# Optimization experiments

Hardware: AMD Instinct MI355X
Metric: run time of the kernel (lower is better)

## Reference

```python
import jax, jax.numpy as jnp
import numpy as np

DIM = 768
HEADS = 12
HD = DIM // HEADS
SCALE = float(np.sqrt(HD))  # sqrt(dim // num_heads)


def layernorm(x, g, b, eps=1e-5):
    m = jnp.mean(x, axis=-1, keepdims=True)
    v = jnp.var(x, axis=-1, keepdims=True)
    return (x - m) * jax.lax.rsqrt(v + eps) * g + b


def dwconv(x, w, b, pad):
    # x: [B,C,H,W], w: [C,1,kh,kw] depthwise
    y = jax.lax.conv_general_dilated(
        x, w, window_strides=(1, 1), padding=[(pad, pad), (pad, pad)],
        feature_group_count=x.shape[1], dimension_numbers=('NCHW', 'OIHW', 'NCHW'))
    return y + b[None, :, None, None]


def mha(xq, xkv, wq, bq, wk, bk, wv, bv, wo, bo):
    # per-head Linears batched over heads; wq/wk/wv: [H, C, hd], biases [H, hd]
    B, N, C = xq.shape
    q = jnp.einsum('bnc,hcd->bhnd', xq, wq) + bq[None, :, None, :]
    k = jnp.einsum('bnc,hcd->bhnd', xkv, wk) + bk[None, :, None, :]
    v = jnp.einsum('bnc,hcd->bhnd', xkv, wv) + bv[None, :, None, :]
    z = jax.nn.sigmoid(jnp.einsum('bhnd,bhmd->bhnm', q, k) / SCALE)  # sigmoid, not softmax
    o = jnp.einsum('bhnm,bhmd->bhnd', z, v)
    o = o.transpose(0, 2, 1, 3).reshape(B, N, C)  # concat heads along feature dim
    return o @ wo + bo


def reference(decoder, wq1, bq1, wk1, bk1, wv1, bv1, wo1, bo1,
              wq2, bq2, wk2, bk2, wv2, bv2, wo2, bo2,
              alphas1, alphas2, peg_w, peg_b,
              ln1_g, ln1_b, ln2_g, ln2_b,
              cn_dw_w, cn_dw_b, cn_ln_g, cn_ln_b,
              cn_w1, cn_b1, cn_w2, cn_b2, cn_scale, cn_alphas):
    B, C, H, W = decoder.shape
    x = decoder.transpose(0, 2, 3, 1).reshape(B, H * W, C)  # [B,N,C]
    # block 1: alpha * x + MHA(x,x,x)
    x = alphas1 * x + mha(x, x, wq1, bq1, wk1, bk1, wv1, bv1, wo1, bo1)
    # PEG: depthwise 3x3 conv (replaces x, no residual in source)
    x4 = x.reshape(B, H, W, C).transpose(0, 3, 1, 2)
    x4 = dwconv(x4, peg_w, peg_b, pad=1)
    x = x4.transpose(0, 2, 3, 1).reshape(B, H * W, C)
    x = layernorm(x, ln1_g, ln1_b)
    # block 2 (encoder is None -> self-attention)
    x = alphas2 * x + mha(x, x, wq2, bq2, wk2, bk2, wv2, bv2, wo2, bo2)
    x = layernorm(x, ln2_g, ln2_b)
    x4 = x.reshape(B, H, W, C).transpose(0, 3, 1, 2)  # [B,C,H,W]
    # CNBlock head: dwconv7x7 -> LN -> Linear(4d) -> GELU -> Linear(d), layer_scale + alpha residual
    y = dwconv(x4, cn_dw_w, cn_dw_b, pad=3)
    y = y.transpose(0, 2, 3, 1)  # [B,H,W,C]
    y = layernorm(y, cn_ln_g, cn_ln_b)
    y = jax.nn.gelu(y @ cn_w1 + cn_b1, approximate=False)
    y = y @ cn_w2 + cn_b2
    y = y.transpose(0, 3, 1, 2)  # [B,C,H,W]
    out = cn_scale[None, :, None, None] * y + x4 * cn_alphas[None, :, None, None]
    return out


def setup_inputs() -> dict:
    key = jax.random.key(0)
    ks = iter(jax.random.split(key, 40))
    def n(shape, s=0.02):
        return jax.random.normal(next(ks), shape, dtype=jnp.float32) * s
    d = {}
    d['decoder'] = jax.random.normal(next(ks), (8, DIM, 32, 32), dtype=jnp.float32)
    for i in (1, 2):
        d[f'wq{i}'] = n((HEADS, DIM, HD)); d[f'bq{i}'] = n((HEADS, HD), 1e-6)
        d[f'wk{i}'] = n((HEADS, DIM, HD)); d[f'bk{i}'] = n((HEADS, HD), 1e-6)
        d[f'wv{i}'] = n((HEADS, DIM, HD)); d[f'bv{i}'] = n((HEADS, HD), 1e-6)
        d[f'wo{i}'] = n((DIM, DIM)); d[f'bo{i}'] = n((DIM,), 1e-6)
    d['alphas1'] = jnp.ones((DIM,), jnp.float32)
    d['alphas2'] = jnp.ones((DIM,), jnp.float32)
    d['peg_w'] = n((DIM, 1, 3, 3), 0.1); d['peg_b'] = n((DIM,), 1e-6)
    d['ln1_g'] = jnp.ones((DIM,), jnp.float32); d['ln1_b'] = jnp.zeros((DIM,), jnp.float32)
    d['ln2_g'] = jnp.ones((DIM,), jnp.float32); d['ln2_b'] = jnp.zeros((DIM,), jnp.float32)
    d['cn_dw_w'] = n((DIM, 1, 7, 7), 0.1); d['cn_dw_b'] = n((DIM,), 0.02)
    d['cn_ln_g'] = jnp.ones((DIM,), jnp.float32); d['cn_ln_b'] = jnp.zeros((DIM,), jnp.float32)
    d['cn_w1'] = n((DIM, 4 * DIM)); d['cn_b1'] = n((4 * DIM,), 0.02)
    d['cn_w2'] = n((4 * DIM, DIM)); d['cn_b2'] = n((DIM,), 0.02)
    d['cn_scale'] = jnp.full((DIM,), 1e-6, jnp.float32)
    d['cn_alphas'] = jnp.ones((DIM,), jnp.float32)
    return d
```

## Files before the change

kernel.cpp:

```cpp
#include <hip/hip_runtime.h>
#include <math.h>

#define BATCH 8
#define CDIM 768
#define NTOK 1024
#define NH 12
#define HDIM 64

typedef __attribute__((ext_vector_type(8))) short bf16x8;
typedef __attribute__((ext_vector_type(4))) float f32x4;

__device__ inline short f2bf(float f) {
    union { float f; unsigned u; } v; v.f = f;
    unsigned r = (v.u + 0x7FFF + ((v.u >> 16) & 1)) >> 16;
    return (short)r;
}

__device__ inline void async_copy16(const short* g, short* l) {
    __builtin_amdgcn_global_load_lds(
        (const __attribute__((address_space(1))) void*)g,
        (__attribute__((address_space(3))) void*)l, 16, 0, 0);
}

__global__ void k_transpose_in(const float* __restrict__ dec, float* __restrict__ x,
                               short* __restrict__ xb) {
    __shared__ float tile[32][33];
    int b = blockIdx.z;
    int n0 = blockIdx.x * 32;
    int c0 = blockIdx.y * 32;
    int tx = threadIdx.x, ty = threadIdx.y;
#pragma unroll
    for (int r = 0; r < 4; ++r) {
        int c = c0 + ty + r * 8;
        tile[ty + r * 8][tx] = dec[((size_t)b * CDIM + c) * NTOK + n0 + tx];
    }
    __syncthreads();
#pragma unroll
    for (int r = 0; r < 4; ++r) {
        int n = n0 + ty + r * 8;
        float val = tile[tx][ty + r * 8];
        size_t idx = ((size_t)b * NTOK + n) * CDIM + c0 + tx;
        x[idx] = val;
        xb[idx] = f2bf(val);
    }
}

__global__ void k_wtrans(const float* __restrict__ src, short* __restrict__ dst,
                         int R, int C) {
    __shared__ float tile[32][33];
    int c0 = blockIdx.x * 32, r0 = blockIdx.y * 32;
    int tx = threadIdx.x, ty = threadIdx.y;
#pragma unroll
    for (int p = 0; p < 4; ++p)
        tile[ty + p * 8][tx] = src[(size_t)(r0 + ty + p * 8) * C + c0 + tx];
    __syncthreads();
#pragma unroll
    for (int p = 0; p < 4; ++p)
        dst[(size_t)(c0 + ty + p * 8) * R + r0 + tx] = f2bf(tile[tx][ty + p * 8]);
}

__global__ __launch_bounds__(256) void k_packqkv(
    const float* __restrict__ wq1, const float* __restrict__ wk1, const float* __restrict__ wv1,
    const float* __restrict__ wq2, const float* __restrict__ wk2, const float* __restrict__ wv2,
    short* __restrict__ dst1, short* __restrict__ dst2) {
    __shared__ float tile[64][65];
    int z = blockIdx.y;
    int set = z / 36, rem = z % 36, sect = rem / 12, h = rem % 12;
    const float* srcs[6] = {wq1, wk1, wv1, wq2, wk2, wv2};
    const float* src = srcs[set * 3 + sect] + (size_t)h * 768 * 64;
    short* dst = (set ? dst2 : dst1) + ((size_t)sect * 768 + h * 64) * 768;
    int k0 = blockIdx.x * 64;
    int t = threadIdx.x;
#pragma unroll
    for (int p = 0; p < 16; ++p) {
        int gid = t + p * 256;
        int r = gid >> 6, c = gid & 63;
        tile[r][c] = src[(size_t)(k0 + r) * 64 + c];
    }
    __syncthreads();
#pragma unroll
    for (int p = 0; p < 16; ++p) {
        int gid = t + p * 256;
        int d = gid >> 6, kk = gid & 63;
        dst[(size_t)d * 768 + k0 + kk] = f2bf(tile[kk][d]);
    }
}

__global__ void k_packbias(const float* __restrict__ bq1, const float* __restrict__ bk1,
                           const float* __restrict__ bv1, const float* __restrict__ bq2,
                           const float* __restrict__ bk2, const float* __restrict__ bv2,
                           float* __restrict__ d1, float* __restrict__ d2) {
    int tid = blockIdx.x * 256 + threadIdx.x;
    if (tid >= 4608) return;
    int set = tid / 2304, n = tid % 2304;
    int sect = n / 768, rem = n % 768;
    const float* srcs[6] = {bq1, bk1, bv1, bq2, bk2, bv2};
    float v = srcs[set * 3 + sect][rem];
    (set ? d2 : d1)[n] = v;
}

#define GM_PLAIN 0
#define GM_PROJ  1
#define GM_GELU  2
#define GM_QKV   3
#define QKVSEC ((size_t)BATCH * NH * NTOK * HDIM)

template<int MODE, int BN>
__global__ __launch_bounds__(256) void k_gemm_mfma(
    const short* __restrict__ A, const short* __restrict__ Bt,
    const float* __restrict__ bias, const float* __restrict__ resid,
    const float* __restrict__ rscale, float* __restrict__ outF,
    short* __restrict__ outB, int M, int N, int K) {
    constexpr int NT = BN / 32;
    constexpr int BP = BN / 64;
    __shared__ short As[2 * 128 * 32];
    __shared__ short Bs[2 * BN * 32];
    int t = threadIdx.x;
    int w = t >> 6, lane = t & 63, l15 = lane & 15, quad = lane >> 4;
    int r0 = blockIdx.x * 128, n0 = blockIdx.y * BN;
    int wr = (w >> 1) * 64, wc = (w & 1) * (BN / 2);
    f32x4 acc[4][NT];
#pragma unroll
    for (int i = 0; i < 4; ++i)
#pragma unroll
        for (int j = 0; j < NT; ++j) acc[i][j] = (f32x4){0.f, 0.f, 0.f, 0.f};
    int sr = t >> 2, sc = (t & 3) * 8;
    const short* Ag = A + (size_t)(r0 + sr) * K + sc;
    const short* Bg = Bt + (size_t)(n0 + sr) * K + sc;
    short* AsW = As + w * 512;
    short* BsW = Bs + w * 512;
    for (int k0 = 0; k0 < K; k0 += 64) {
        __syncthreads();
#pragma unroll
        for (int c = 0; c < 2; ++c) {
#pragma unroll
            for (int p = 0; p < 2; ++p)
                async_copy16(Ag + k0 + c * 32 + (size_t)p * 64 * K,
                             AsW + c * 4096 + p * 2048);
#pragma unroll
            for (int p = 0; p < BP; ++p)
                async_copy16(Bg + k0 + c * 32 + (size_t)p * 64 * K,
                             BsW + c * (BN * 32) + p * 2048);
        }
        __syncthreads();
#pragma unroll
        for (int c = 0; c < 2; ++c) {
            bf16x8 af[4], bf[NT];
#pragma unroll
            for (int i = 0; i < 4; ++i)
                af[i] = *(const bf16x8*)&As[c * 4096 + (wr + i * 16 + l15) * 32 + quad * 8];
#pragma unroll
            for (int j = 0; j < NT; ++j)
                bf[j] = *(const bf16x8*)&Bs[c * (BN * 32) + (wc + j * 16 + l15) * 32 + quad * 8];
#pragma unroll
            for (int i = 0; i < 4; ++i)
#pragma unroll
                for (int j = 0; j < NT; ++j)
                    acc[i][j] = __builtin_amdgcn_mfma_f32_16x16x32_bf16(af[i], bf[j], acc[i][j], 0, 0, 0);
        }
    }
#pragma unroll
    for (int i = 0; i < 4; ++i)
#pragma unroll
        for (int j = 0; j < NT; ++j)
#pragma unroll
            for (int rr = 0; rr < 4; ++rr) {
                int row = r0 + wr + i * 16 + quad * 4 + rr;
                int col = n0 + wc + j * 16 + l15;
                float val = acc[i][j][rr] + bias[col];
                if (MODE == GM_PROJ) {
                    val += rscale[col] * resid[(size_t)row * N + col];
                    outF[(size_t)row * N + col] = val;
                } else if (MODE == GM_GELU) {
                    float u = val * (1.0f + 0.044715f * val * val);
                    float zz = __builtin_amdgcn_rcpf(
                        1.0f + __builtin_amdgcn_exp2f(-2.3022082f * u));
                    outB[(size_t)row * N + col] = f2bf(val * zz);
                } else if (MODE == GM_PLAIN) {
                    outF[(size_t)row * N + col] = val;
                } else {
                    int sect = col / 768, rem = col - sect * 768;
                    int hh = rem >> 6, d = rem & 63;
                    int bb = row >> 10, tok = row & 1023;
                    outB[(size_t)sect * QKVSEC +
                         (((size_t)bb * NH + hh) * NTOK + tok) * HDIM + d] = f2bf(val);
                }
            }
}

__global__ __launch_bounds__(256) void k_attn_mfma(
    const short* __restrict__ q, const short* __restrict__ k,
    const short* __restrict__ v, short* __restrict__ o) {
    __shared__ short Ks[64][72];
    __shared__ short Vt[64][72];
    __shared__ short Ps[128][72];
    int b = blockIdx.z, h = blockIdx.y;
    int q0 = blockIdx.x * 128;
    int t = threadIdx.x;
    int w = t >> 6, lane = t & 63, l15 = lane & 15, quad = lane >> 4;
    size_t base = ((size_t)(b * NH + h)) * NTOK * HDIM;
    const short* qp = q + base;
    const short* kp = k + base;
    const short* vp = v + base;
    bf16x8 qf[2][2];
#pragma unroll
    for (int mt = 0; mt < 2; ++mt)
#pragma unroll
        for (int kc = 0; kc < 2; ++kc)
            qf[mt][kc] = *(const bf16x8*)&qp[(size_t)(q0 + w * 32 + mt * 16 + l15) * HDIM + kc * 32 + quad * 8];
    f32x4 oacc[2][4];
#pragma unroll
    for (int mt = 0; mt < 2; ++mt)
#pragma unroll
        for (int dt = 0; dt < 4; ++dt) oacc[mt][dt] = (f32x4){0.f, 0.f, 0.f, 0.f};
    for (int kt = 0; kt < 16; ++kt) {
        __syncthreads();
#pragma unroll
        for (int p = 0; p < 2; ++p) {
            int gid = t + p * 256;
            int r = gid >> 3, c8 = (gid & 7) * 8;
            *(bf16x8*)&Ks[r][c8] = *(const bf16x8*)&kp[(size_t)(kt * 64 + r) * HDIM + c8];
        }
#pragma unroll
        for (int p = 0; p < 2; ++p) {
            int tok = t & 63, d0 = (t >> 6) * 8 + p * 32;
            bf16x8 vv = *(const bf16x8*)&vp[(size_t)(kt * 64 + tok) * HDIM + d0];
#pragma unroll
            for (int j = 0; j < 8; ++j) Vt[d0 + j][tok] = vv[j];
        }
        __syncthreads();
        f32x4 sacc[2][4];
#pragma unroll
        for (int mt = 0; mt < 2; ++mt)
#pragma unroll
            for (int nt = 0; nt < 4; ++nt) sacc[mt][nt] = (f32x4){0.f, 0.f, 0.f, 0.f};
#pragma unroll
        for (int nt = 0; nt < 4; ++nt) {
            bf16x8 kf0 = *(const bf16x8*)&Ks[nt * 16 + l15][quad * 8];
            bf16x8 kf1 = *(const bf16x8*)&Ks[nt * 16 + l15][32 + quad * 8];
#pragma unroll
            for (int mt = 0; mt < 2; ++mt) {
                sacc[mt][nt] = __builtin_amdgcn_mfma_f32_16x16x32_bf16(qf[mt][0], kf0, sacc[mt][nt], 0, 0, 0);
                sacc[mt][nt] = __builtin_amdgcn_mfma_f32_16x16x32_bf16(qf[mt][1], kf1, sacc[mt][nt], 0, 0, 0);
            }
        }
#pragma unroll
        for (int mt = 0; mt < 2; ++mt)
#pragma unroll
            for (int nt = 0; nt < 4; ++nt)
#pragma unroll
                for (int rr = 0; rr < 4; ++rr) {
                    float s = sacc[mt][nt][rr];
                    float z = __builtin_amdgcn_rcpf(
                        1.0f + __builtin_amdgcn_exp2f(s * -0.18033688011112042f));
                    Ps[w * 32 + mt * 16 + quad * 4 + rr][nt * 16 + l15] = f2bf(z);
                }
        __syncthreads();
        bf16x8 vfr[2][4];
#pragma unroll
        for (int kc = 0; kc < 2; ++kc)
#pragma unroll
            for (int dt = 0; dt < 4; ++dt)
                vfr[kc][dt] = *(const bf16x8*)&Vt[dt * 16 + l15][kc * 32 + quad * 8];
#pragma unroll
        for (int mt = 0; mt < 2; ++mt)
#pragma unroll
            for (int kc = 0; kc < 2; ++kc) {
                bf16x8 pf = *(const bf16x8*)&Ps[w * 32 + mt * 16 + l15][kc * 32 + quad * 8];
#pragma unroll
                for (int dt = 0; dt < 4; ++dt)
                    oacc[mt][dt] = __builtin_amdgcn_mfma_f32_16x16x32_bf16(pf, vfr[kc][dt], oacc[mt][dt], 0, 0, 0);
            }
    }
#pragma unroll
    for (int mt = 0; mt < 2; ++mt)
#pragma unroll
        for (int dt = 0; dt < 4; ++dt)
#pragma unroll
            for (int rr = 0; rr < 4; ++rr) {
                int tok = q0 + w * 32 + mt * 16 + quad * 4 + rr;
                int c = h * 64 + dt * 16 + l15;
                o[((size_t)b * NTOK + tok) * CDIM + c] = f2bf(oacc[mt][dt][rr]);
            }
}

template<int K>
__global__ __launch_bounds__(256) void k_dwconv_t(
    const float* __restrict__ in, const float* __restrict__ w,
    const float* __restrict__ bias, float* __restrict__ out) {
    constexpr int PAD = K / 2;
    constexpr int KK = K * K;
    int t = threadIdx.x;
    int c = blockIdx.y * 64 + (t & 63);
    int j = blockIdx.x * 4 + (t >> 6);
    int b = blockIdx.z;
    float wr[KK];
#pragma unroll
    for (int qq = 0; qq < KK; ++qq) wr[qq] = w[(size_t)c * KK + qq];
    float bsv = bias[c];
    const float* base = in + (size_t)b * NTOK * CDIM + c;
    float win[K][K];
#pragma unroll
    for (int s = 1; s < K; ++s) {
        int ii = s - 1 - PAD;
#pragma unroll
        for (int qq = 0; qq < K; ++qq) {
            int jj = j - PAD + qq;
            win[s][qq] = (ii >= 0 && jj >= 0 && jj < 32)
                         ? base[(size_t)(ii * 32 + jj) * CDIM] : 0.0f;
        }
    }
#pragma unroll
    for (int i = 0; i < 32; ++i) {
#pragma unroll
        for (int r = 0; r < K - 1; ++r)
#pragma unroll
            for (int qq = 0; qq < K; ++qq) win[r][qq] = win[r + 1][qq];
        int ii = i + PAD;
#pragma unroll
        for (int qq = 0; qq < K; ++qq) {
            int jj = j - PAD + qq;
            win[K - 1][qq] = (ii < 32 && jj >= 0 && jj < 32)
                             ? base[(size_t)(ii * 32 + jj) * CDIM] : 0.0f;
        }
        float acc = bsv;
#pragma unroll
        for (int r = 0; r < K; ++r)
#pragma unroll
            for (int qq = 0; qq < K; ++qq)
                acc = fmaf(win[r][qq], wr[r * K + qq], acc);
        out[((size_t)b * NTOK + i * 32 + j) * CDIM + c] = acc;
    }
}

__global__ __launch_bounds__(256) void k_ln(
    const float* __restrict__ in, const float* __restrict__ g,
    const float* __restrict__ b, float* __restrict__ outF, short* __restrict__ outB) {
    int row = blockIdx.x;
    const float* xr = in + (size_t)row * CDIM;
    int t = threadIdx.x;
    float x0 = xr[t], x1 = xr[t + 256], x2 = xr[t + 512];
    float s = x0 + x1 + x2;
    float sq = x0 * x0 + x1 * x1 + x2 * x2;
#pragma unroll
    for (int off = 32; off > 0; off >>= 1) {
        s += __shfl_down(s, off);
        sq += __shfl_down(sq, off);
    }
    __shared__ float ws[4], wq2[4];
    int wid = t >> 6, lane = t & 63;
    if (lane == 0) { ws[wid] = s; wq2[wid] = sq; }
    __syncthreads();
    if (t == 0) {
        float S = ws[0] + ws[1] + ws[2] + ws[3];
        float Q = wq2[0] + wq2[1] + wq2[2] + wq2[3];
        float m = S * (1.0f / CDIM);
        float var = Q * (1.0f / CDIM) - m * m;
        ws[0] = m;
        wq2[0] = rsqrtf(var + 1e-5f);
    }
    __syncthreads();
    float m = ws[0], inv = wq2[0];
    float y0 = (x0 - m) * inv * g[t] + b[t];
    float y1 = (x1 - m) * inv * g[t + 256] + b[t + 256];
    float y2 = (x2 - m) * inv * g[t + 512] + b[t + 512];
    if (outF) {
        float* orow = outF + (size_t)row * CDIM;
        orow[t] = y0; orow[t + 256] = y1; orow[t + 512] = y2;
    }
    if (outB) {
        short* orow = outB + (size_t)row * CDIM;
        orow[t] = f2bf(y0); orow[t + 256] = f2bf(y1); orow[t + 512] = f2bf(y2);
    }
}

__global__ void k_final(const float* __restrict__ y, const float* __restrict__ xln,
                        const float* __restrict__ scale, const float* __restrict__ alph,
                        float* __restrict__ out) {
    __shared__ float tile[32][33];
    int b = blockIdx.z, n0 = blockIdx.x * 32, c0 = blockIdx.y * 32;
    int tx = threadIdx.x, ty = threadIdx.y;
#pragma unroll
    for (int r = 0; r < 4; ++r) {
        int n = n0 + ty + r * 8, c = c0 + tx;
        size_t idx = ((size_t)b * NTOK + n) * CDIM + c;
        tile[tx][ty + r * 8] = scale[c] * y[idx] + alph[c] * xln[idx];
    }
    __syncthreads();
#pragma unroll
    for (int r = 0; r < 4; ++r) {
        int c = c0 + ty + r * 8;
        out[((size_t)b * CDIM + c) * NTOK + n0 + tx] = tile[ty + r * 8][tx];
    }
}

extern "C" void kernel_launch(void* const* d_in, const int* in_sizes, int n_in,
                              void* d_out, int out_size, void* d_ws, size_t ws_size,
                              hipStream_t stream) {
    const float* dec = (const float*)d_in[0];
    const float* wq1 = (const float*)d_in[1]; const float* bq1 = (const float*)d_in[2];
    const float* wk1 = (const float*)d_in[3]; const float* bk1 = (const float*)d_in[4];
    const float* wv1 = (const float*)d_in[5]; const float* bv1 = (const float*)d_in[6];
    const float* wo1 = (const float*)d_in[7]; const float* bo1 = (const float*)d_in[8];
    const float* wq2 = (const float*)d_in[9]; const float* bq2 = (const float*)d_in[10];
    const float* wk2 = (const float*)d_in[11]; const float* bk2 = (const float*)d_in[12];
    const float* wv2 = (const float*)d_in[13]; const float* bv2 = (const float*)d_in[14];
    const float* wo2 = (const float*)d_in[15]; const float* bo2 = (const float*)d_in[16];
    const float* alphas1 = (const float*)d_in[17];
    const float* alphas2 = (const float*)d_in[18];
    const float* peg_w = (const float*)d_in[19]; const float* peg_b = (const float*)d_in[20];
    const float* ln1_g = (const float*)d_in[21]; const float* ln1_b = (const float*)d_in[22];
    const float* ln2_g = (const float*)d_in[23]; const float* ln2_b = (const float*)d_in[24];
    const float* cn_dw_w = (const float*)d_in[25]; const float* cn_dw_b = (const float*)d_in[26];
    const float* cn_ln_g = (const float*)d_in[27]; const float* cn_ln_b = (const float*)d_in[28];
    const float* cn_w1 = (const float*)d_in[29]; const float* cn_b1 = (const float*)d_in[30];
    const float* cn_w2 = (const float*)d_in[31]; const float* cn_b2 = (const float*)d_in[32];
    const float* cn_scale = (const float*)d_in[33]; const float* cn_alphas = (const float*)d_in[34];
    float* out = (float*)d_out;

    const size_t S = (size_t)BATCH * NTOK * CDIM;
    float* A0 = (float*)d_ws;
    float* A1 = A0 + S;
    short* Xb  = (short*)(A1 + S);
    short* QKV = Xb + S;
    short* Ob  = QKV + 3 * S;
    short* Hb  = Ob + S;
    short* Wqkv1 = Hb + 2 * S;
    short* Wqkv2 = Wqkv1 + 2304 * 768;
    short* WoT1  = Wqkv2 + 2304 * 768;
    short* WoT2  = WoT1 + 768 * 768;
    short* W1T   = WoT2 + 768 * 768;
    short* W2T   = W1T + (size_t)3072 * 768;
    float* bqkv1 = (float*)(W2T + (size_t)768 * 3072);
    float* bqkv2 = bqkv1 + 2304;
    float* yF    = (float*)QKV;
    short* Hfull = QKV + 2 * S;

    dim3 tb(32, 8);
    dim3 dwgrid(8, 12, 8);

    k_packqkv<<<dim3(12, 72), 256, 0, stream>>>(wq1, wk1, wv1, wq2, wk2, wv2, Wqkv1, Wqkv2);
    k_wtrans<<<dim3(24, 24), tb, 0, stream>>>(wo1, WoT1, 768, 768);
    k_wtrans<<<dim3(24, 24), tb, 0, stream>>>(wo2, WoT2, 768, 768);
    k_wtrans<<<dim3(96, 24), tb, 0, stream>>>(cn_w1, W1T, 768, 3072);
    k_wtrans<<<dim3(24, 96), tb, 0, stream>>>(cn_w2, W2T, 3072, 768);
    k_packbias<<<18, 256, 0, stream>>>(bq1, bk1, bv1, bq2, bk2, bv2, bqkv1, bqkv2);

    k_transpose_in<<<dim3(32, 24, 8), tb, 0, stream>>>(dec, A0, Xb);

    k_gemm_mfma<GM_QKV, 128><<<dim3(64, 18), 256, 0, stream>>>(
        Xb, Wqkv1, bqkv1, nullptr, nullptr, nullptr, QKV, 8192, 2304, 768);
    k_attn_mfma<<<dim3(8, 12, 8), 256, 0, stream>>>(QKV, QKV + S, QKV + 2 * S, Ob);
    k_gemm_mfma<GM_PROJ, 64><<<dim3(64, 12), 256, 0, stream>>>(
        Ob, WoT1, bo1, A0, alphas1, A1, nullptr, 8192, 768, 768);
    k_dwconv_t<3><<<dwgrid, 256, 0, stream>>>(A1, peg_w, peg_b, A0);
    k_ln<<<8192, 256, 0, stream>>>(A0, ln1_g, ln1_b, A1, Xb);

    k_gemm_mfma<GM_QKV, 128><<<dim3(64, 18), 256, 0, stream>>>(
        Xb, Wqkv2, bqkv2, nullptr, nullptr, nullptr, QKV, 8192, 2304, 768);
    k_attn_mfma<<<dim3(8, 12, 8), 256, 0, stream>>>(QKV, QKV + S, QKV + 2 * S, Ob);
    k_gemm_mfma<GM_PROJ, 64><<<dim3(64, 12), 256, 0, stream>>>(
        Ob, WoT2, bo2, A1, alphas2, A0, nullptr, 8192, 768, 768);
    k_ln<<<8192, 256, 0, stream>>>(A0, ln2_g, ln2_b, A1, nullptr);

    k_dwconv_t<7><<<dwgrid, 256, 0, stream>>>(A1, cn_dw_w, cn_dw_b, A0);
    k_ln<<<8192, 256, 0, stream>>>(A0, cn_ln_g, cn_ln_b, nullptr, Xb);
    k_gemm_mfma<GM_GELU, 128><<<dim3(64, 24), 256, 0, stream>>>(
        Xb, W1T, cn_b1, nullptr, nullptr, nullptr, Hfull, 8192, 3072, 768);
    k_gemm_mfma<GM_PLAIN, 64><<<dim3(64, 12), 256, 0, stream>>>(
        Hfull, W2T, cn_b2, nullptr, nullptr, yF, nullptr, 8192, 768, 3072);
    k_final<<<dim3(32, 24, 8), tb, 0, stream>>>(yF, A1, cn_scale, cn_alphas, out);
}
```

Before: 655.4 us.

## Fuse final residual and NCHW transpose into last GEMM; widen QKV/GELU tiles

The final CNBlock residual (layer-scale times GEMM output plus alpha times the LN output) and the NHWC-to-NCHW transpose move into the epilogue of the second MLP GEMM. That epilogue stages the tile through shared memory and writes coalesced float4 rows, which removes the separate k_final kernel and the fp32 intermediate round trip. The QKV and first MLP GEMMs also switch to 256-wide N tiles, which doubles per-thread accumulators and increases register pressure in exchange for more operand reuse and fewer blocks.

After: 734.6 us. 12.1% more time.

```diff
diff --git a/kernel.cpp b/kernel.cpp
--- a/kernel.cpp
+++ b/kernel.cpp
@@ -99,7 +99,7 @@
     (set ? d2 : d1)[n] = v;
 }
 
-#define GM_PLAIN 0
+#define GM_FINAL 0
 #define GM_PROJ  1
 #define GM_GELU  2
 #define GM_QKV   3
@@ -109,12 +109,16 @@
 __global__ __launch_bounds__(256) void k_gemm_mfma(
     const short* __restrict__ A, const short* __restrict__ Bt,
     const float* __restrict__ bias, const float* __restrict__ resid,
-    const float* __restrict__ rscale, float* __restrict__ outF,
-    short* __restrict__ outB, int M, int N, int K) {
+    const float* __restrict__ rscale, const float* __restrict__ alph,
+    float* __restrict__ outF, short* __restrict__ outB, int M, int N, int K) {
     constexpr int NT = BN / 32;
     constexpr int BP = BN / 64;
-    __shared__ short As[2 * 128 * 32];
-    __shared__ short Bs[2 * BN * 32];
+    constexpr int STAGE = 2 * 128 * 32 + 2 * BN * 32;
+    constexpr int FINALS = (MODE == GM_FINAL) ? 64 * 132 * 2 : 0;
+    constexpr int SMEM = STAGE > FINALS ? STAGE : FINALS;
+    __shared__ short smem[SMEM];
+    short* As = smem;
+    short* Bs = smem + 2 * 128 * 32;
     int t = threadIdx.x;
     int w = t >> 6, lane = t & 63, l15 = lane & 15, quad = lane >> 4;
     int r0 = blockIdx.x * 128, n0 = blockIdx.y * BN;
@@ -158,6 +162,31 @@
                 for (int j = 0; j < NT; ++j)
                     acc[i][j] = __builtin_amdgcn_mfma_f32_16x16x32_bf16(af[i], bf[j], acc[i][j], 0, 0, 0);
         }
+    }
+    if (MODE == GM_FINAL) {
+        __syncthreads();
+        float* T = (float*)smem;
+#pragma unroll
+        for (int i = 0; i < 4; ++i)
+#pragma unroll
+            for (int j = 0; j < NT; ++j)
+#pragma unroll
+                for (int rr = 0; rr < 4; ++rr) {
+                    int rl = wr + i * 16 + quad * 4 + rr;
+                    int cl = wc + j * 16 + l15;
+                    int row = r0 + rl, col = n0 + cl;
+                    float val = acc[i][j][rr] + bias[col];
+                    val = rscale[col] * val + alph[col] * resid[(size_t)row * N + col];
+                    T[cl * 132 + rl] = val;
+                }
+        __syncthreads();
+        int c = t >> 2, qo = (t & 3) * 32;
+        int b = r0 >> 10, tokbase = r0 & 1023;
+        float* obase = outF + ((size_t)(b * 768 + n0 + c)) * 1024 + tokbase + qo;
+#pragma unroll
+        for (int ii = 0; ii < 8; ++ii)
+            *(float4*)&obase[ii * 4] = *(float4*)&T[c * 132 + qo + ii * 4];
+        return;
     }
 #pragma unroll
     for (int i = 0; i < 4; ++i)
@@ -176,8 +205,6 @@
                     float zz = __builtin_amdgcn_rcpf(
                         1.0f + __builtin_amdgcn_exp2f(-2.3022082f * u));
                     outB[(size_t)row * N + col] = f2bf(val * zz);
-                } else if (MODE == GM_PLAIN) {
-                    outF[(size_t)row * N + col] = val;
                 } else {
                     int sect = col / 768, rem = col - sect * 768;
                     int hh = rem >> 6, d = rem & 63;
@@ -371,26 +398,6 @@
     if (outB) {
         short* orow = outB + (size_t)row * CDIM;
         orow[t] = f2bf(y0); orow[t + 256] = f2bf(y1); orow[t + 512] = f2bf(y2);
-    }
-}
-
-__global__ void k_final(const float* __restrict__ y, const float* __restrict__ xln,
-                        const float* __restrict__ scale, const float* __restrict__ alph,
-                        float* __restrict__ out) {
-    __shared__ float tile[32][33];
-    int b = blockIdx.z, n0 = blockIdx.x * 32, c0 = blockIdx.y * 32;
-    int tx = threadIdx.x, ty = threadIdx.y;
-#pragma unroll
-    for (int r = 0; r < 4; ++r) {
-        int n = n0 + ty + r * 8, c = c0 + tx;
-        size_t idx = ((size_t)b * NTOK + n) * CDIM + c;
-        tile[tx][ty + r * 8] = scale[c] * y[idx] + alph[c] * xln[idx];
-    }
-    __syncthreads();
-#pragma unroll
-    for (int r = 0; r < 4; ++r) {
-        int c = c0 + ty + r * 8;
-        out[((size_t)b * CDIM + c) * NTOK + n0 + tx] = tile[ty + r * 8][tx];
     }
 }
 
@@ -433,7 +440,6 @@
     short* W2T   = W1T + (size_t)3072 * 768;
     float* bqkv1 = (float*)(W2T + (size_t)768 * 3072);
     float* bqkv2 = bqkv1 + 2304;
-    float* yF    = (float*)QKV;
     short* Hfull = QKV + 2 * S;
 
     dim3 tb(32, 8);
@@ -448,26 +454,25 @@
 
     k_transpose_in<<<dim3(32, 24, 8), tb, 0, stream>>>(dec, A0, Xb);
 
-    k_gemm_mfma<GM_QKV, 128><<<dim3(64, 18), 256, 0, stream>>>(
-        Xb, Wqkv1, bqkv1, nullptr, nullptr, nullptr, QKV, 8192, 2304, 768);
+    k_gemm_mfma<GM_QKV, 256><<<dim3(64, 9), 256, 0, stream>>>(
+        Xb, Wqkv1, bqkv1, nullptr, nullptr, nullptr, nullptr, QKV, 8192, 2304, 768);
     k_attn_mfma<<<dim3(8, 12, 8), 256, 0, stream>>>(QKV, QKV + S, QKV + 2 * S, Ob);
     k_gemm_mfma<GM_PROJ, 64><<<dim3(64, 12), 256, 0, stream>>>(
-        Ob, WoT1, bo1, A0, alphas1, A1, nullptr, 8192, 768, 768);
+        Ob, WoT1, bo1, A0, alphas1, nullptr, A1, nullptr, 8192, 768, 768);
     k_dwconv_t<3><<<dwgrid, 256, 0, stream>>>(A1, peg_w, peg_b, A0);
     k_ln<<<8192, 256, 0, stream>>>(A0, ln1_g, ln1_b, A1, Xb);
 
-    k_gemm_mfma<GM_QKV, 128><<<dim3(64, 18), 256, 0, stream>>>(
-        Xb, Wqkv2, bqkv2, nullptr, nullptr, nullptr, QKV, 8192, 2304, 768);
+    k_gemm_mfma<GM_QKV, 256><<<dim3(64, 9), 256, 0, stream>>>(
+        Xb, Wqkv2, bqkv2, nullptr, nullptr, nullptr, nullptr, QKV, 8192, 2304, 768);
     k_attn_mfma<<<dim3(8, 12, 8), 256, 0, stream>>>(QKV, QKV + S, QKV + 2 * S, Ob);
     k_gemm_mfma<GM_PROJ, 64><<<dim3(64, 12), 256, 0, stream>>>(
-        Ob, WoT2, bo2, A1, alphas2, A0, nullptr, 8192, 768, 768);
+        Ob, WoT2, bo2, A1, alphas2, nullptr, A0, nullptr, 8192, 768, 768);
     k_ln<<<8192, 256, 0, stream>>>(A0, ln2_g, ln2_b, A1, nullptr);
 
     k_dwconv_t<7><<<dwgrid, 256, 0, stream>>>(A1, cn_dw_w, cn_dw_b, A0);
     k_ln<<<8192, 256, 0, stream>>>(A0, cn_ln_g, cn_ln_b, nullptr, Xb);
-    k_gemm_mfma<GM_GELU, 128><<<dim3(64, 24), 256, 0, stream>>>(
-        Xb, W1T, cn_b1, nullptr, nullptr, nullptr, Hfull, 8192, 3072, 768);
-    k_gemm_mfma<GM_PLAIN, 64><<<dim3(64, 12), 256, 0, stream>>>(
-        Hfull, W2T, cn_b2, nullptr, nullptr, yF, nullptr, 8192, 768, 3072);
-    k_final<<<dim3(32, 24, 8), tb, 0, stream>>>(yF, A1, cn_scale, cn_alphas, out);
-}
+    k_gemm_mfma<GM_GELU, 256><<<dim3(64, 12), 256, 0, stream>>>(
+        Xb, W1T, cn_b1, nullptr, nullptr, nullptr, nullptr, Hfull, 8192, 3072, 768);
+    k_gemm_mfma<GM_FINAL, 64><<<dim3(64, 12), 256, 0, stream>>>(
+        Hfull, W2T, cn_b2, A1, cn_scale, cn_alphas, out, nullptr, 8192, 768, 3072);
+}
```
